# Performance work log

Hardware: AMD Instinct MI355X
Metric: run time of the kernel (lower is better)

## Reference

```python
import jax, jax.numpy as jnp
import numpy as np
from jax import lax

H = 20  # hidden_size


def _rnn_layer(x_seq, h0, W_ih, W_hh, b_ih, b_hh):
    """Vanilla tanh RNN layer. x_seq: [B,T,D], h0: [B,H]. Returns ([B,T,H], [B,H])."""
    # Precompute input projection for all timesteps (the only large GEMM).
    xp = jnp.einsum('btd,hd->bth', x_seq, W_ih) + b_ih + b_hh  # [B,T,H]

    def step(h, xt):
        h = jnp.tanh(xt + h @ W_hh.T)
        return h, h

    h_last, hs = lax.scan(step, h0, jnp.swapaxes(xp, 0, 1))  # hs: [T,B,H]
    return jnp.swapaxes(hs, 0, 1), h_last


def setup_inputs() -> dict:
    key = jax.random.key(0)
    ks = jax.random.split(key, 12)
    B, T = 4096, 512
    s = 1.0 / np.sqrt(H)  # PyTorch default uniform(-1/sqrt(H), 1/sqrt(H))
    u = lambda k, shape: jax.random.uniform(k, shape, jnp.float32, -s, s)
    return {
        'x': jax.random.normal(ks[0], (B, T, 1), jnp.float32),
        'hidden': jax.random.normal(ks[1], (2, B, H), jnp.float32),
        'W_ih0': u(ks[2], (H, 1)),
        'W_hh0': u(ks[3], (H, H)),
        'b_ih0': u(ks[4], (H,)),
        'b_hh0': u(ks[5], (H,)),
        'W_ih1': u(ks[6], (H, H)),
        'W_hh1': u(ks[7], (H, H)),
        'b_ih1': u(ks[8], (H,)),
        'b_hh1': u(ks[9], (H,)),
        'fc_w': u(ks[10], (1, H)),
        'fc_b': u(ks[11], (1,)),
    }


def reference(x, hidden, W_ih0, W_hh0, b_ih0, b_hh0, W_ih1, W_hh1, b_ih1, b_hh1, fc_w, fc_b):
    # 2-layer vanilla RNN (eval mode: inter-layer dropout disabled)
    h0_seq, h0_last = _rnn_layer(x, hidden[0], W_ih0, W_hh0, b_ih0, b_hh0)
    h1_seq, h1_last = _rnn_layer(h0_seq, hidden[1], W_ih1, W_hh1, b_ih1, b_hh1)
    out = h1_seq[:, -1, :] @ fc_w.T + fc_b  # [B,1]
    new_hidden = jnp.stack([h0_last, h1_last], axis=0)  # [2,B,H]
    return out, new_hidden
```

## Files before the change

### kernel.cpp

```cpp
#include <hip/hip_runtime.h>


#define Bsz 4096
#define Tn  512
#define Hn  20
#define GB  3
#define K   8
#define RING 16
#define NPH (Tn / K)
#define XPAD 520
#define NTHREADS 128

typedef float v2 __attribute__((ext_vector_type(2)));

__device__ __forceinline__ float tanh_fast(float v) {
    float e = __expf(2.0f * v);
    return 1.0f - 2.0f * __builtin_amdgcn_rcpf(e + 1.0f);
}

#define DOT20P(acc, accb, W, H) do { \
    acc  = __builtin_elementwise_fma(W##0, H##0, acc);  \
    accb = __builtin_elementwise_fma(W##1, H##1, accb); \
    acc  = __builtin_elementwise_fma(W##2, H##2, acc);  \
    accb = __builtin_elementwise_fma(W##3, H##3, accb); \
    acc  = __builtin_elementwise_fma(W##4, H##4, acc);  \
    accb = __builtin_elementwise_fma(W##5, H##5, accb); \
    acc  = __builtin_elementwise_fma(W##6, H##6, acc);  \
    accb = __builtin_elementwise_fma(W##7, H##7, accb); \
    acc  = __builtin_elementwise_fma(W##8, H##8, acc);  \
    accb = __builtin_elementwise_fma(W##9, H##9, accb); \
} while (0)

#define LOAD_ROWP(W, ptr) \
    v2 W##0, W##1, W##2, W##3, W##4, W##5, W##6, W##7, W##8, W##9; \
    { const float4* _p = (const float4*)(ptr); \
      float4 _t; \
      _t = _p[0]; W##0 = (v2){_t.x, _t.y}; W##1 = (v2){_t.z, _t.w}; \
      _t = _p[1]; W##2 = (v2){_t.x, _t.y}; W##3 = (v2){_t.z, _t.w}; \
      _t = _p[2]; W##4 = (v2){_t.x, _t.y}; W##5 = (v2){_t.z, _t.w}; \
      _t = _p[3]; W##6 = (v2){_t.x, _t.y}; W##7 = (v2){_t.z, _t.w}; \
      _t = _p[4]; W##8 = (v2){_t.x, _t.y}; W##9 = (v2){_t.z, _t.w}; }

#define READ_H(H, base) \
    v2 H##0, H##1, H##2, H##3, H##4, H##5, H##6, H##7, H##8, H##9; \
    { const float4 _a = *(const float4*)((base) + 0);  \
      const float4 _b = *(const float4*)((base) + 4);  \
      const float4 _c = *(const float4*)((base) + 8);  \
      const float4 _d = *(const float4*)((base) + 12); \
      const float4 _e = *(const float4*)((base) + 16); \
      H##0 = (v2){_a.x, _a.y}; H##1 = (v2){_a.z, _a.w}; \
      H##2 = (v2){_b.x, _b.y}; H##3 = (v2){_b.z, _b.w}; \
      H##4 = (v2){_c.x, _c.y}; H##5 = (v2){_c.z, _c.w}; \
      H##6 = (v2){_d.x, _d.y}; H##7 = (v2){_d.z, _d.w}; \
      H##8 = (v2){_e.x, _e.y}; H##9 = (v2){_e.z, _e.w}; }

__global__ __launch_bounds__(NTHREADS)
__attribute__((amdgpu_waves_per_eu(1, 4)))
void rnn2_fused(const float* __restrict__ x,
                const float* __restrict__ hidden,
                const float* __restrict__ W_ih0,
                const float* __restrict__ W_hh0,
                const float* __restrict__ b_ih0,
                const float* __restrict__ b_hh0,
                const float* __restrict__ W_ih1,
                const float* __restrict__ W_hh1,
                const float* __restrict__ b_ih1,
                const float* __restrict__ b_hh1,
                const float* __restrict__ fc_w,
                const float* __restrict__ fc_b,
                float* __restrict__ out)
{
    const int tid  = threadIdx.x;
    const int wave = tid >> 6;
    const int lane = tid & 63;
    int g = lane / Hn;
    int j = lane - g * Hn;
    const bool lane_ok = (lane < GB * Hn);
    if (!lane_ok) { g = GB - 1; j = lane - 60; }

    const int  b        = blockIdx.x * GB + g;
    const bool b_ok     = (b < Bsz);
    const int  bl       = b_ok ? b : (Bsz - 1);
    const bool store_ok = lane_ok && b_ok;

    __shared__ float xs[GB][XPAD];
    __shared__ float h0r[RING][GB][Hn];
    __shared__ float h1s[GB][Hn];

    const float* rowA = (wave == 0) ? (W_hh0 + j * Hn) : (W_ih1 + j * Hn);
    LOAD_ROWP(wA, rowA)
    LOAD_ROWP(wB, W_hh1 + j * Hn)

    const float wih0  = W_ih0[j];
    const float bias0 = b_ih0[j] + b_hh0[j];
    const float bias1 = b_ih1[j] + b_hh1[j];

    {
        const int bB = blockIdx.x * GB;
        #pragma unroll
        for (int r = 0; r < (GB * Tn) / (NTHREADS * 4); ++r) {
            const int c  = (r * NTHREADS + tid) * 4;
            const int gg = c >> 9;
            const int t  = c & (Tn - 1);
            const int bb = (bB + gg < Bsz) ? (bB + gg) : (Bsz - 1);
            float4 v = *(const float4*)(x + (long)bb * Tn + t);
            *(float4*)&xs[gg][t] = v;
        }
    }

    if (wave == 0) h0r[RING - 1][g][j] = hidden[bl * Hn + j];
    else           h1s[g][j]           = hidden[(long)Bsz * Hn + bl * Hn + j];
    __syncthreads();

    float n_keep = 0.f;

    for (int k = 0; k <= NPH; ++k) {
        if (wave == 0) {
            if (k < NPH) {
                #pragma unroll
                for (int u = 0; u < K; ++u) {
                    const int t = k * K + u;
                    READ_H(hA, &h0r[(t - 1) & (RING - 1)][g][0])
                    const float xt = xs[g][t];
                    v2 a  = (v2){fmaf(xt, wih0, bias0), 0.f};
                    v2 ab = (v2){0.f, 0.f};
                    DOT20P(a, ab, wA, hA);
                    const v2 s = a + ab;
                    const float n = tanh_fast(s.x + s.y);
                    h0r[t & (RING - 1)][g][j] = n;
                    n_keep = n;
                }
            }
        } else {
            if (k > 0) {
                #pragma unroll
                for (int u = 0; u < K; ++u) {
                    const int t = (k - 1) * K + u;
                    READ_H(hA, &h0r[t & (RING - 1)][g][0])
                    READ_H(hB, &h1s[g][0])
                    v2 a1  = (v2){bias1, 0.f};
                    v2 a1b = (v2){0.f, 0.f};
                    v2 a2  = (v2){0.f, 0.f};
                    v2 a2b = (v2){0.f, 0.f};
                    DOT20P(a1, a1b, wA, hA);
                    DOT20P(a2, a2b, wB, hB);
                    const v2 s = (a1 + a1b) + (a2 + a2b);
                    const float n = tanh_fast(s.x + s.y);
                    h1s[g][j] = n;
                    n_keep = n;
                }
            }
        }
        if (k < NPH) __syncthreads();
    }

    if (wave == 0) {
        if (store_ok)
            out[Bsz + (long)b * Hn + j] = n_keep;
    } else {
        if (store_ok) {
            out[Bsz + (long)Bsz * Hn + (long)b * Hn + j] = n_keep;
            if (j == 0) {
                LOAD_ROWP(fw, fc_w)
                READ_H(hv, &h1s[g][0])
                v2 aA = (v2){fc_b[0], 0.f};
                v2 aB = (v2){0.f, 0.f};
                DOT20P(aA, aB, fw, hv);
                const v2 sf = aA + aB;
                out[b] = sf.x + sf.y;
            }
        }
    }
}

extern "C" void kernel_launch(void* const* d_in, const int* in_sizes, int n_in,
                              void* d_out, int out_size, void* d_ws, size_t ws_size,
                              hipStream_t stream) {
    const float* x      = (const float*)d_in[0];
    const float* hidden = (const float*)d_in[1];
    const float* W_ih0  = (const float*)d_in[2];
    const float* W_hh0  = (const float*)d_in[3];
    const float* b_ih0  = (const float*)d_in[4];
    const float* b_hh0  = (const float*)d_in[5];
    const float* W_ih1  = (const float*)d_in[6];
    const float* W_hh1  = (const float*)d_in[7];
    const float* b_ih1  = (const float*)d_in[8];
    const float* b_hh1  = (const float*)d_in[9];
    const float* fc_w   = (const float*)d_in[10];
    const float* fc_b   = (const float*)d_in[11];

    const int nblocks = (Bsz + GB - 1) / GB;
    rnn2_fused<<<nblocks, NTHREADS, 0, stream>>>(
        x, hidden, W_ih0, W_hh0, b_ih0, b_hh0,
        W_ih1, W_hh1, b_ih1, b_hh1, fc_w, fc_b, (float*)d_out);
}
```

Measured before the change: 128.1 us.

## Process eight sequences per block with three hidden rows per lane

Each block now handles 8 batch sequences instead of 3. Each lane computes 3 hidden units (rows jj, jj+8 and a clamped jj+16) for one sequence, instead of 1 unit per lane. The aim is to cut block count, barrier and LDS-read overhead per sequence, and to give each lane three independent dot-product chains of ILP per timestep. In exchange, occupancy drops to one wave per SIMD, register use rises, some lanes do duplicate work on the clamped row, and the bounds guards are gone because 4096 divides evenly by 8.

```diff
diff --git a/kernel.cpp b/kernel.cpp
--- a/kernel.cpp
+++ b/kernel.cpp
@@ -4,11 +4,11 @@
 #define Bsz 4096
 #define Tn  512
 #define Hn  20
-#define GB  3
+#define GB  8
 #define K   8
 #define RING 16
 #define NPH (Tn / K)
-#define XPAD 520
+#define XPAD 516
 #define NTHREADS 128
 
 typedef float v2 __attribute__((ext_vector_type(2)));
@@ -55,7 +55,7 @@
       H##8 = (v2){_e.x, _e.y}; H##9 = (v2){_e.z, _e.w}; }
 
 __global__ __launch_bounds__(NTHREADS)
-__attribute__((amdgpu_waves_per_eu(1, 4)))
+__attribute__((amdgpu_waves_per_eu(1, 1)))
 void rnn2_fused(const float* __restrict__ x,
                 const float* __restrict__ hidden,
                 const float* __restrict__ W_ih0,
@@ -73,27 +73,29 @@
     const int tid  = threadIdx.x;
     const int wave = tid >> 6;
     const int lane = tid & 63;
-    int g = lane / Hn;
-    int j = lane - g * Hn;
-    const bool lane_ok = (lane < GB * Hn);
-    if (!lane_ok) { g = GB - 1; j = lane - 60; }
-
-    const int  b        = blockIdx.x * GB + g;
-    const bool b_ok     = (b < Bsz);
-    const int  bl       = b_ok ? b : (Bsz - 1);
-    const bool store_ok = lane_ok && b_ok;
+    const int g    = lane >> 3;
+    const int jj   = lane & 7;
+    const int r0   = jj;
+    const int r1   = jj + 8;
+    const int r2   = (jj + 16 < Hn) ? (jj + 16) : (Hn - 1);
+    const int b    = blockIdx.x * GB + g;
 
     __shared__ float xs[GB][XPAD];
     __shared__ float h0r[RING][GB][Hn];
     __shared__ float h1s[GB][Hn];
 
-    const float* rowA = (wave == 0) ? (W_hh0 + j * Hn) : (W_ih1 + j * Hn);
-    LOAD_ROWP(wA, rowA)
-    LOAD_ROWP(wB, W_hh1 + j * Hn)
-
-    const float wih0  = W_ih0[j];
-    const float bias0 = b_ih0[j] + b_hh0[j];
-    const float bias1 = b_ih1[j] + b_hh1[j];
+    const float* mA = (wave == 0) ? W_hh0 : W_ih1;
+    LOAD_ROWP(wA0, mA + r0 * Hn)
+    LOAD_ROWP(wA1, mA + r1 * Hn)
+    LOAD_ROWP(wA2, mA + r2 * Hn)
+    LOAD_ROWP(wB0, W_hh1 + r0 * Hn)
+    LOAD_ROWP(wB1, W_hh1 + r1 * Hn)
+    LOAD_ROWP(wB2, W_hh1 + r2 * Hn)
+
+    const float wih0_0 = W_ih0[r0], wih0_1 = W_ih0[r1], wih0_2 = W_ih0[r2];
+    const float bA0 = (wave == 0) ? (b_ih0[r0] + b_hh0[r0]) : (b_ih1[r0] + b_hh1[r0]);
+    const float bA1 = (wave == 0) ? (b_ih0[r1] + b_hh0[r1]) : (b_ih1[r1] + b_hh1[r1]);
+    const float bA2 = (wave == 0) ? (b_ih0[r2] + b_hh0[r2]) : (b_ih1[r2] + b_hh1[r2]);
 
     {
         const int bB = blockIdx.x * GB;
@@ -102,17 +104,23 @@
             const int c  = (r * NTHREADS + tid) * 4;
             const int gg = c >> 9;
             const int t  = c & (Tn - 1);
-            const int bb = (bB + gg < Bsz) ? (bB + gg) : (Bsz - 1);
-            float4 v = *(const float4*)(x + (long)bb * Tn + t);
+            float4 v = *(const float4*)(x + (long)(bB + gg) * Tn + t);
             *(float4*)&xs[gg][t] = v;
         }
     }
 
-    if (wave == 0) h0r[RING - 1][g][j] = hidden[bl * Hn + j];
-    else           h1s[g][j]           = hidden[(long)Bsz * Hn + bl * Hn + j];
+    if (wave == 0) {
+        h0r[RING - 1][g][r0] = hidden[(long)b * Hn + r0];
+        h0r[RING - 1][g][r1] = hidden[(long)b * Hn + r1];
+        h0r[RING - 1][g][r2] = hidden[(long)b * Hn + r2];
+    } else {
+        h1s[g][r0] = hidden[(long)Bsz * Hn + (long)b * Hn + r0];
+        h1s[g][r1] = hidden[(long)Bsz * Hn + (long)b * Hn + r1];
+        h1s[g][r2] = hidden[(long)Bsz * Hn + (long)b * Hn + r2];
+    }
     __syncthreads();
 
-    float n_keep = 0.f;
+    float k0 = 0.f, k1 = 0.f, k2 = 0.f;
 
     for (int k = 0; k <= NPH; ++k) {
         if (wave == 0) {
@@ -122,13 +130,20 @@
                     const int t = k * K + u;
                     READ_H(hA, &h0r[(t - 1) & (RING - 1)][g][0])
                     const float xt = xs[g][t];
-                    v2 a  = (v2){fmaf(xt, wih0, bias0), 0.f};
-                    v2 ab = (v2){0.f, 0.f};
-                    DOT20P(a, ab, wA, hA);
-                    const v2 s = a + ab;
-                    const float n = tanh_fast(s.x + s.y);
-                    h0r[t & (RING - 1)][g][j] = n;
-                    n_keep = n;
+                    v2 a0 = (v2){fmaf(xt, wih0_0, bA0), 0.f}, a0b = (v2){0.f, 0.f};
+                    v2 a1 = (v2){fmaf(xt, wih0_1, bA1), 0.f}, a1b = (v2){0.f, 0.f};
+                    v2 a2 = (v2){fmaf(xt, wih0_2, bA2), 0.f}, a2b = (v2){0.f, 0.f};
+                    DOT20P(a0, a0b, wA0, hA);
+                    DOT20P(a1, a1b, wA1, hA);
+                    DOT20P(a2, a2b, wA2, hA);
+                    const v2 s0 = a0 + a0b, s1 = a1 + a1b, s2 = a2 + a2b;
+                    k0 = tanh_fast(s0.x + s0.y);
+                    k1 = tanh_fast(s1.x + s1.y);
+                    k2 = tanh_fast(s2.x + s2.y);
+                    const int q = t & (RING - 1);
+                    h0r[q][g][r0] = k0;
+                    h0r[q][g][r1] = k1;
+                    h0r[q][g][r2] = k2;
                 }
             }
         } else {
@@ -138,16 +153,27 @@
                     const int t = (k - 1) * K + u;
                     READ_H(hA, &h0r[t & (RING - 1)][g][0])
                     READ_H(hB, &h1s[g][0])
-                    v2 a1  = (v2){bias1, 0.f};
-                    v2 a1b = (v2){0.f, 0.f};
-                    v2 a2  = (v2){0.f, 0.f};
-                    v2 a2b = (v2){0.f, 0.f};
-                    DOT20P(a1, a1b, wA, hA);
-                    DOT20P(a2, a2b, wB, hB);
-                    const v2 s = (a1 + a1b) + (a2 + a2b);
-                    const float n = tanh_fast(s.x + s.y);
-                    h1s[g][j] = n;
-                    n_keep = n;
+                    v2 a0 = (v2){bA0, 0.f}, a0b = (v2){0.f, 0.f};
+                    v2 a1 = (v2){bA1, 0.f}, a1b = (v2){0.f, 0.f};
+                    v2 a2 = (v2){bA2, 0.f}, a2b = (v2){0.f, 0.f};
+                    v2 c0 = (v2){0.f, 0.f}, c0b = (v2){0.f, 0.f};
+                    v2 c1 = (v2){0.f, 0.f}, c1b = (v2){0.f, 0.f};
+                    v2 c2 = (v2){0.f, 0.f}, c2b = (v2){0.f, 0.f};
+                    DOT20P(a0, a0b, wA0, hA);
+                    DOT20P(a1, a1b, wA1, hA);
+                    DOT20P(a2, a2b, wA2, hA);
+                    DOT20P(c0, c0b, wB0, hB);
+                    DOT20P(c1, c1b, wB1, hB);
+                    DOT20P(c2, c2b, wB2, hB);
+                    const v2 s0 = (a0 + a0b) + (c0 + c0b);
+                    const v2 s1 = (a1 + a1b) + (c1 + c1b);
+                    const v2 s2 = (a2 + a2b) + (c2 + c2b);
+                    k0 = tanh_fast(s0.x + s0.y);
+                    k1 = tanh_fast(s1.x + s1.y);
+                    k2 = tanh_fast(s2.x + s2.y);
+                    h1s[g][r0] = k0;
+                    h1s[g][r1] = k1;
+                    h1s[g][r2] = k2;
                 }
             }
         }
@@ -155,20 +181,21 @@
     }
 
     if (wave == 0) {
-        if (store_ok)
-            out[Bsz + (long)b * Hn + j] = n_keep;
+        out[Bsz + (long)b * Hn + r0] = k0;
+        out[Bsz + (long)b * Hn + r1] = k1;
+        out[Bsz + (long)b * Hn + r2] = k2;
     } else {
-        if (store_ok) {
-            out[Bsz + (long)Bsz * Hn + (long)b * Hn + j] = n_keep;
-            if (j == 0) {
-                LOAD_ROWP(fw, fc_w)
-                READ_H(hv, &h1s[g][0])
-                v2 aA = (v2){fc_b[0], 0.f};
-                v2 aB = (v2){0.f, 0.f};
-                DOT20P(aA, aB, fw, hv);
-                const v2 sf = aA + aB;
-                out[b] = sf.x + sf.y;
-            }
+        out[Bsz + (long)Bsz * Hn + (long)b * Hn + r0] = k0;
+        out[Bsz + (long)Bsz * Hn + (long)b * Hn + r1] = k1;
+        out[Bsz + (long)Bsz * Hn + (long)b * Hn + r2] = k2;
+        if (jj == 0) {
+            LOAD_ROWP(fw, fc_w)
+            READ_H(hv, &h1s[g][0])
+            v2 aA = (v2){fc_b[0], 0.f};
+            v2 aB = (v2){0.f, 0.f};
+            DOT20P(aA, aB, fw, hv);
+            const v2 s = aA + aB;
+            out[b] = s.x + s.y;
         }
     }
 }
@@ -189,8 +216,7 @@
     const float* fc_w   = (const float*)d_in[10];
     const float* fc_b   = (const float*)d_in[11];
 
-    const int nblocks = (Bsz + GB - 1) / GB;
-    rnn2_fused<<<nblocks, NTHREADS, 0, stream>>>(
+    rnn2_fused<<<Bsz / GB, NTHREADS, 0, stream>>>(
         x, hidden, W_ih0, W_hh0, b_ih0, b_hh0,
         W_ih1, W_hh1, b_ih1, b_hh1, fc_w, fc_b, (float*)d_out);
 }
```

Result: no change. 127.7 us (median of 2 runs) (-0.3%).
